# Performance work log

Measured on AMD Instinct MI355X. Metric: run time of the kernel, lower is better.

The kernel has to match this reference:

```python
import jax, jax.numpy as jnp
import numpy as np

B, S, D, H, E, O = 8, 2048, 512, 8, 64, 512  # batch, seq, d_in, heads, head_dim, out_dim
NEG_INF = -1e9  # keras Attention adds -1e9 to masked scores


def setup_inputs() -> dict:
    key = jax.random.key(0)
    kq, kk, kv, ko, kx = jax.random.split(key, 5)
    # glorot-uniform-style scale for kernel_size=1 convs (fan_in=D, fan_out=E)
    sqkv = float(np.sqrt(6.0 / (D + E)))
    so = float(np.sqrt(6.0 / (H * E + O)))
    return {
        "query": jax.random.normal(kx, (B, S, D), dtype=jnp.float32),
        "Wq": jax.random.uniform(kq, (H, D, E), jnp.float32, -sqkv, sqkv),
        "Wk": jax.random.uniform(kk, (H, D, E), jnp.float32, -sqkv, sqkv),
        "Wv": jax.random.uniform(kv, (H, D, E), jnp.float32, -sqkv, sqkv),
        "Wo": jax.random.uniform(ko, (H * E, O), jnp.float32, -so, so),
    }


def reference(query, Wq, Wk, Wv, Wo):
    # value defaults to query (self-attention). Conv1D(kernel_size=1, no bias)
    # is a per-timestep linear map; all heads batched into one einsum.
    Q = jnp.einsum('bsd,hde->bhse', query, Wq)
    K = jnp.einsum('bsd,hde->bhse', query, Wk)
    V = jnp.einsum('bsd,hde->bhse', query, Wv)
    # keras Attention(use_scale=False, causal=True): scores = Q K^T (no scale)
    scores = jnp.einsum('bhse,bhte->bhst', Q, K)
    causal = jnp.tril(jnp.ones((S, S), dtype=bool))  # [S, S]
    scores = jnp.where(causal, scores, NEG_INF)
    attn = jax.nn.softmax(scores, axis=-1)
    ctx = jnp.einsum('bhst,bhte->bhse', attn, V)  # [B, H, S, E]
    # concat heads along last axis (head-major), then 1x1 conv projection
    ctx = ctx.transpose(0, 2, 1, 3).reshape(B, S, H * E)
    return jnp.einsum('bsf,fo->bso', ctx, Wo)
```

## Files before the change

kernel.cpp:

```cpp
#include <hip/hip_runtime.h>
#include <stdint.h>

#define Bb 8
#define Ss 2048
#define Dd 512
#define Hh 8
#define Ee 64
#define Oo 512
#define Ff 512
#define Ncat 1536

typedef _Float16 half_t;
typedef __attribute__((ext_vector_type(8))) _Float16 f16x8;
typedef __attribute__((ext_vector_type(4))) float f32x4;
typedef __attribute__((ext_vector_type(16))) float f32x16;
typedef __attribute__((ext_vector_type(4))) float f4;
typedef __attribute__((ext_vector_type(4))) half_t h16x4;
typedef __attribute__((ext_vector_type(4))) unsigned int u32x4;

__device__ __forceinline__ float exp2_fast(float x) {
    float r; asm("v_exp_f32 %0, %1" : "=v"(r) : "v"(x)); return r;
}
__device__ __forceinline__ f32x16 zero16() {
    f32x16 z;
#pragma unroll
    for (int i = 0; i < 16; ++i) z[i] = 0.f;
    return z;
}
__device__ __forceinline__ void gload16(const half_t* g, half_t* l) {
    __builtin_amdgcn_global_load_lds(
        (const __attribute__((address_space(1))) void*)g,
        (__attribute__((address_space(3))) void*)l, 16, 0, 0);
}

__global__ __launch_bounds__(256) void k_cvt_x(const float* __restrict__ x,
                                               half_t* __restrict__ xh) {
    int t = blockIdx.x * 256 + threadIdx.x;
    int s = t >> 6, c = t & 63;
    int cg = c >> 3, cl = c & 7;
    const float* src = x + (size_t)s * Dd + c * 8;
    f4 v0 = *(const f4*)src;
    f4 v1 = *(const f4*)(src + 4);
    union { half_t h[8]; u32x4 u; } o;
#pragma unroll
    for (int j = 0; j < 4; ++j) { o.h[j] = (half_t)v0[j]; o.h[4 + j] = (half_t)v1[j]; }
    int cd = cg * 8 + (cl ^ (s & 7));
    *(u32x4*)(xh + (size_t)s * Dd + cd * 8) = o.u;
}

__global__ __launch_bounds__(256) void k_cvt_w(const float* __restrict__ Wq, const float* __restrict__ Wk,
                                               const float* __restrict__ Wv, const float* __restrict__ Wo,
                                               half_t* __restrict__ Wcat, half_t* __restrict__ WoT) {
    int t = blockIdx.x * 256 + threadIdx.x;
    union { half_t h[8]; u32x4 u; } o;
    if (t < Ncat * 64) {
        int n = t >> 6, dc = t & 63;
        int sel = n >> 9, h = (n >> 6) & 7, e = n & 63;
        const float* W = (sel == 0) ? Wq : (sel == 1) ? Wk : Wv;
        const float* src = W + ((size_t)h * Dd + dc * 8) * Ee + e;
#pragma unroll
        for (int j = 0; j < 8; ++j) o.h[j] = (half_t)src[(size_t)j * Ee];
        int dcs = (dc & ~7) | ((dc & 7) ^ (n & 7));
        *(u32x4*)(Wcat + (size_t)n * Dd + dcs * 8) = o.u;
    } else {
        int u2 = t - Ncat * 64;
        int oo = u2 >> 6, fc = u2 & 63;
        const float* src = Wo + (size_t)(fc * 8) * Oo + oo;
#pragma unroll
        for (int j = 0; j < 8; ++j) o.h[j] = (half_t)src[(size_t)j * Oo];
        int fcs = (fc & ~7) | ((fc & 7) ^ (oo & 7));
        *(u32x4*)(WoT + (size_t)oo * Ff + fcs * 8) = o.u;
    }
}

__global__ __launch_bounds__(256, 2) void k_qkv(const half_t* __restrict__ A,
                                                const half_t* __restrict__ Bw,
                                                half_t* __restrict__ Q,
                                                half_t* __restrict__ K,
                                                half_t* __restrict__ Vt) {
    __shared__ __attribute__((aligned(16))) half_t S[32768];

    int bid = blockIdx.x;
    int virt = (bid & 7) * 192 + (bid >> 3);
    int bm = virt / 12, bn = virt % 12;
    int m0 = bm * 128, n0 = bn * 128;

    int wave = threadIdx.x >> 6, lane = threadIdx.x & 63;
    int ar = lane & 15, kg = lane >> 4;
    int wm = wave >> 1, wn = wave & 1;
    int lr = lane >> 3, lc = lane & 7;

    f32x4 acc[4][4];
#pragma unroll
    for (int i = 0; i < 4; ++i)
#pragma unroll
        for (int j = 0; j < 4; ++j) acc[i][j] = (f32x4){0, 0, 0, 0};

#define STAGE_QKV(buf, kt)                                                                   \
    {                                                                                        \
        _Pragma("unroll")                                                                    \
        for (int i = 0; i < 4; ++i) {                                                        \
            int seg = wave * 4 + i;                                                          \
            int row = seg * 8 + lr;                                                          \
            gload16(A  + (size_t)(m0 + row) * Dd + (kt) * 64 + lc * 8,                       \
                    S + (buf) * 8192 + seg * 512);                                           \
            gload16(Bw + (size_t)(n0 + row) * Dd + (kt) * 64 + lc * 8,                       \
                    S + 16384 + (buf) * 8192 + seg * 512);                                   \
        }                                                                                    \
    }

    STAGE_QKV(0, 0);
    __syncthreads();
    int cur = 0;
    for (int kt = 0; kt < 8; ++kt) {
        if (kt < 7) STAGE_QKV(cur ^ 1, kt + 1);
        f16x8 bf[4][2];
#pragma unroll
        for (int n = 0; n < 4; ++n) {
            int row = wn * 64 + n * 16 + ar;
#pragma unroll
            for (int kh = 0; kh < 2; ++kh)
                bf[n][kh] = *(const f16x8*)&S[16384 + cur * 8192 + row * 64 + (((kg + kh * 4)) ^ (row & 7)) * 8];
        }
#pragma unroll
        for (int mi = 0; mi < 4; ++mi) {
            int row = wm * 64 + mi * 16 + ar;
            f16x8 a0 = *(const f16x8*)&S[cur * 8192 + row * 64 + ((kg)     ^ (row & 7)) * 8];
            f16x8 a1 = *(const f16x8*)&S[cur * 8192 + row * 64 + ((kg + 4) ^ (row & 7)) * 8];
#pragma unroll
            for (int n = 0; n < 4; ++n) {
                acc[mi][n] = __builtin_amdgcn_mfma_f32_16x16x32_f16(a0, bf[n][0], acc[mi][n], 0, 0, 0);
                acc[mi][n] = __builtin_amdgcn_mfma_f32_16x16x32_f16(a1, bf[n][1], acc[mi][n], 0, 0, 0);
            }
        }
        __syncthreads();
        cur ^= 1;
    }
    int sel = n0 >> 9;
    if (sel < 2) {
#pragma unroll
        for (int sn = 0; sn < 4; ++sn) {
            int nb = n0 + wn * 64 + sn * 16;
            int h = (nb >> 6) & 7, eb = nb & 63;
#pragma unroll
            for (int mi = 0; mi < 4; ++mi)
#pragma unroll
                for (int r = 0; r < 4; ++r) {
                    int sg = m0 + wm * 64 + mi * 16 + kg * 4 + r;
                    int bh = (sg >> 11) * 8 + h, sl = sg & 2047;
                    half_t val = (half_t)acc[mi][sn][r];
                    if (sel == 0) Q[((size_t)bh * Ss + sl) * Ee + eb + ar] = val;
                    else          K[((size_t)bh * Ss + sl) * Ee + eb + ar] = val;
                }
        }
    } else {
#pragma unroll
        for (int sn = 0; sn < 4; ++sn) {
            int e_loc = wn * 64 + sn * 16 + ar;
#pragma unroll
            for (int mi = 0; mi < 4; ++mi)
#pragma unroll
                for (int r = 0; r < 4; ++r) {
                    int s_loc = wm * 64 + mi * 16 + kg * 4 + r;
                    S[e_loc * 136 + s_loc] = (half_t)acc[mi][sn][r];
                }
        }
        __syncthreads();
        int b = m0 >> 11, sbase = m0 & 2047;
#pragma unroll
        for (int i = 0; i < 8; ++i) {
            int e_loc = wave * 32 + i * 4 + (lane >> 4);
            int chunk = lane & 15;
            f16x8 v = *(const f16x8*)&S[e_loc * 136 + chunk * 8];
            int h = ((n0 >> 6) + (e_loc >> 6)) & 7;
            int e_in = e_loc & 63;
            int bh = b * 8 + h;
            *(f16x8*)(Vt + ((size_t)bh * Ee + e_in) * Ss + sbase + chunk * 8) = v;
        }
    }
#undef STAGE_QKV
}

__global__ __launch_bounds__(256, 4) void k_attn(const half_t* __restrict__ Q,
                                                 const half_t* __restrict__ Kg,
                                                 const half_t* __restrict__ Vtg,
                                                 half_t* __restrict__ ctx) {
    __shared__ __attribute__((aligned(16))) half_t Klds[2][64 * 64];
    __shared__ __attribute__((aligned(16))) half_t Vlds[2][64 * 64];

    int bid = blockIdx.x;
    int xcd = bid & 7;
    int idx = bid >> 3;
    int g   = idx >> 3;
    int g0 = g & 3, j = g >> 2;
    int qb;
    switch (j) {
        case 0:  qb = 15 - g0; break;
        case 1:  qb = 8 + (g0 ^ 2); break;
        case 2:  qb = 4 + g0; break;
        default: qb = g0 ^ 1; break;
    }
    int bh  = xcd * 8 + (idx & 7);

    int wave = threadIdx.x >> 6, lane = threadIdx.x & 63;
    int ql = lane & 31, hi = lane >> 5;
    int qt32 = qb * 4 + wave;
    int qg = qt32 * 32 + ql;

    const half_t* Qb = Q   + (size_t)bh * Ss * Ee;
    const half_t* Kb = Kg  + (size_t)bh * Ss * Ee;
    const half_t* Vb = Vtg + (size_t)bh * Ee * Ss;

    const half_t* qp = Qb + (size_t)qg * Ee + hi * 8;
    f16x8 qf[4];
    const half_t l2e = (half_t)1.44269504f;
#pragma unroll
    for (int d = 0; d < 4; ++d) {
        qf[d] = *(const f16x8*)(qp + d * 16);
#pragma unroll
        for (int jj = 0; jj < 8; ++jj) qf[d][jj] *= l2e;
    }

    f32x16 ot0 = zero16(), ot1 = zero16();
    float m = -1e30f, lp = 0.f;

#define STAGE_KV(buf, kt64)                                                                 \
    {                                                                                       \
        _Pragma("unroll")                                                                   \
        for (int c = 0; c < 2; ++c) {                                                       \
            int seg = 2 * wave + c;                                                         \
            int tK = seg >> 2, dK = seg & 3;                                                \
            gload16(Kb + ((size_t)(kt64) * 64 + tK * 32 + ql) * Ee + dK * 16 + hi * 8,      \
                    &Klds[buf][seg * 512]);                                                 \
            int eh = (seg >> 1) & 1, d2 = seg & 1;                                          \
            gload16(Vb + (size_t)(eh * 32 + ql) * Ss + (kt64) * 64 + tK * 32 + d2 * 16 + hi * 8, \
                    &Vlds[buf][seg * 512]);                                                 \
        }                                                                                   \
    }

    STAGE_KV(0, 0);
    int cur = 0;
    int ktmax64 = qb * 2 + 1;
    for (int kt64 = 0; kt64 <= ktmax64; ++kt64) {
        __syncthreads();
        if (kt64 < ktmax64) STAGE_KV(cur ^ 1, kt64 + 1);
        int j0 = kt64 * 2;
        if (j0 <= qt32) {
            f32x16 s0 = zero16(), s1 = zero16();
            {
                f16x8 ka0 = *(const f16x8*)&Klds[cur][lane * 8];
                f16x8 ka1 = *(const f16x8*)&Klds[cur][512 + lane * 8];
                f16x8 ka2 = *(const f16x8*)&Klds[cur][1024 + lane * 8];
                f16x8 ka3 = *(const f16x8*)&Klds[cur][1536 + lane * 8];
                __builtin_amdgcn_s_setprio(1);
                s0 = __builtin_amdgcn_mfma_f32_32x32x16_f16(ka0, qf[0], s0, 0, 0, 0);
                s0 = __builtin_amdgcn_mfma_f32_32x32x16_f16(ka1, qf[1], s0, 0, 0, 0);
                s0 = __builtin_amdgcn_mfma_f32_32x32x16_f16(ka2, qf[2], s0, 0, 0, 0);
                s0 = __builtin_amdgcn_mfma_f32_32x32x16_f16(ka3, qf[3], s0, 0, 0, 0);
                __builtin_amdgcn_s_setprio(0);
            }
            {
                f16x8 kb0 = *(const f16x8*)&Klds[cur][2048 + lane * 8];
                f16x8 kb1 = *(const f16x8*)&Klds[cur][2560 + lane * 8];
                f16x8 kb2 = *(const f16x8*)&Klds[cur][3072 + lane * 8];
                f16x8 kb3 = *(const f16x8*)&Klds[cur][3584 + lane * 8];
                __builtin_amdgcn_s_setprio(1);
                s1 = __builtin_amdgcn_mfma_f32_32x32x16_f16(kb0, qf[0], s1, 0, 0, 0);
                s1 = __builtin_amdgcn_mfma_f32_32x32x16_f16(kb1, qf[1], s1, 0, 0, 0);
                s1 = __builtin_amdgcn_mfma_f32_32x32x16_f16(kb2, qf[2], s1, 0, 0, 0);
                s1 = __builtin_amdgcn_mfma_f32_32x32x16_f16(kb3, qf[3], s1, 0, 0, 0);
                __builtin_amdgcn_s_setprio(0);
            }
            if (j0 + 1 >= qt32) {
                int sh0 = (j0 - qt32) * 32;
                int sh1 = sh0 + 32;
#pragma unroll
                for (int r = 0; r < 16; ++r) {
                    int kloc = (r & 3) + 8 * (r >> 2) + 4 * hi;
                    if (sh0 >= 0 && kloc + sh0 > ql) s0[r] = -1e30f;
                    if (kloc + sh1 > ql)             s1[r] = -1e30f;
                }
            }
            float mt = fmaxf(s0[0], s1[0]);
#pragma unroll
            for (int r = 1; r < 16; ++r) mt = fmaxf(mt, fmaxf(s0[r], s1[r]));
            mt = fmaxf(mt, __shfl_xor(mt, 32));
            if (!__all(mt <= m + 8.0f)) {
                float mn = fmaxf(m, mt);
                float sc = exp2_fast(m - mn);
#pragma unroll
                for (int r = 0; r < 16; ++r) { ot0[r] *= sc; ot1[r] *= sc; }
                lp *= sc;
                m = mn;
            }
            float rs = 0.f;
#pragma unroll
            for (int r = 0; r < 16; ++r) { s0[r] = exp2_fast(s0[r] - m); rs += s0[r]; }
#pragma unroll
            for (int r = 0; r < 16; ++r) { s1[r] = exp2_fast(s1[r] - m); rs += s1[r]; }
            lp += rs;

            unsigned w0[8], w1[8];
#pragma unroll
            for (int mm = 0; mm < 8; ++mm) {
                asm("v_cvt_pkrtz_f16_f32 %0, %1, %2" : "=v"(w0[mm]) : "v"(s0[2 * mm]), "v"(s0[2 * mm + 1]));
                asm("v_cvt_pkrtz_f16_f32 %0, %1, %2" : "=v"(w1[mm]) : "v"(s1[2 * mm]), "v"(s1[2 * mm + 1]));
            }
            unsigned a0 = (unsigned)__shfl_xor((int)(hi ? w0[0] : w0[2]), 32);
            unsigned a1 = (unsigned)__shfl_xor((int)(hi ? w0[1] : w0[3]), 32);
            unsigned a2 = (unsigned)__shfl_xor((int)(hi ? w0[4] : w0[6]), 32);
            unsigned a3 = (unsigned)__shfl_xor((int)(hi ? w0[5] : w0[7]), 32);
            unsigned b0 = (unsigned)__shfl_xor((int)(hi ? w1[0] : w1[2]), 32);
            unsigned b1 = (unsigned)__shfl_xor((int)(hi ? w1[1] : w1[3]), 32);
            unsigned b2 = (unsigned)__shfl_xor((int)(hi ? w1[4] : w1[6]), 32);
            unsigned b3 = (unsigned)__shfl_xor((int)(hi ? w1[5] : w1[7]), 32);
            union { unsigned u[4]; f16x8 v; } pA0, pA1, pB0, pB1;
            pA0.u[0] = hi ? a0 : w0[0];  pA0.u[1] = hi ? a1 : w0[1];
            pA0.u[2] = hi ? w0[2] : a0;  pA0.u[3] = hi ? w0[3] : a1;
            pA1.u[0] = hi ? a2 : w0[4];  pA1.u[1] = hi ? a3 : w0[5];
            pA1.u[2] = hi ? w0[6] : a2;  pA1.u[3] = hi ? w0[7] : a3;
            pB0.u[0] = hi ? b0 : w1[0];  pB0.u[1] = hi ? b1 : w1[1];
            pB0.u[2] = hi ? w1[2] : b0;  pB0.u[3] = hi ? w1[3] : b1;
            pB1.u[0] = hi ? b2 : w1[4];  pB1.u[1] = hi ? b3 : w1[5];
            pB1.u[2] = hi ? w1[6] : b2;  pB1.u[3] = hi ? w1[7] : b3;

            {
                f16x8 va0 = *(const f16x8*)&Vlds[cur][lane * 8];
                f16x8 va1 = *(const f16x8*)&Vlds[cur][512 + lane * 8];
                f16x8 va2 = *(const f16x8*)&Vlds[cur][1024 + lane * 8];
                f16x8 va3 = *(const f16x8*)&Vlds[cur][1536 + lane * 8];
                __builtin_amdgcn_s_setprio(1);
                ot0 = __builtin_amdgcn_mfma_f32_32x32x16_f16(va0, pA0.v, ot0, 0, 0, 0);
                ot0 = __builtin_amdgcn_mfma_f32_32x32x16_f16(va1, pA1.v, ot0, 0, 0, 0);
                ot1 = __builtin_amdgcn_mfma_f32_32x32x16_f16(va2, pA0.v, ot1, 0, 0, 0);
                ot1 = __builtin_amdgcn_mfma_f32_32x32x16_f16(va3, pA1.v, ot1, 0, 0, 0);
                __builtin_amdgcn_s_setprio(0);
            }
            {
                f16x8 vb0 = *(const f16x8*)&Vlds[cur][2048 + lane * 8];
                f16x8 vb1 = *(const f16x8*)&Vlds[cur][2560 + lane * 8];
                f16x8 vb2 = *(const f16x8*)&Vlds[cur][3072 + lane * 8];
                f16x8 vb3 = *(const f16x8*)&Vlds[cur][3584 + lane * 8];
                __builtin_amdgcn_s_setprio(1);
                ot0 = __builtin_amdgcn_mfma_f32_32x32x16_f16(vb0, pB0.v, ot0, 0, 0, 0);
                ot0 = __builtin_amdgcn_mfma_f32_32x32x16_f16(vb1, pB1.v, ot0, 0, 0, 0);
                ot1 = __builtin_amdgcn_mfma_f32_32x32x16_f16(vb2, pB0.v, ot1, 0, 0, 0);
                ot1 = __builtin_amdgcn_mfma_f32_32x32x16_f16(vb3, pB1.v, ot1, 0, 0, 0);
                __builtin_amdgcn_s_setprio(0);
            }
        }
        cur ^= 1;
    }
#undef STAGE_KV

    float lf = lp + __shfl_xor(lp, 32);
    float inv = 1.0f / lf;
    int b = bh >> 3, h = bh & 7;
    int qs = qg & 7;
    half_t* cb = ctx + ((size_t)b * Ss + qg) * Ff;
#pragma unroll
    for (int gg = 0; gg < 4; ++gg) {
        h16x4 v0, v1;
#pragma unroll
        for (int jj = 0; jj < 4; ++jj) {
            v0[jj] = (half_t)(ot0[gg * 4 + jj] * inv);
            v1[jj] = (half_t)(ot1[gg * 4 + jj] * inv);
        }
        *(h16x4*)(cb + (h * 8 + (gg ^ qs)) * 8 + 4 * hi)       = v0;
        *(h16x4*)(cb + (h * 8 + ((gg + 4) ^ qs)) * 8 + 4 * hi) = v1;
    }
}

__global__ __launch_bounds__(256, 2) void k_proj(const half_t* __restrict__ A,
                                                 const half_t* __restrict__ Bw,
                                                 float* __restrict__ out) {
    __shared__ __attribute__((aligned(16))) half_t Ab[2][128 * 64];
    __shared__ __attribute__((aligned(16))) half_t Bbuf[2][128 * 64];

    int bid = blockIdx.x;
    int virt = (bid & 7) * 64 + (bid >> 3);
    int bm = virt >> 2, bn = virt & 3;
    int m0 = bm * 128, n0 = bn * 128;

    int wave = threadIdx.x >> 6, lane = threadIdx.x & 63;
    int ar = lane & 15, kg = lane >> 4;
    int wm = wave >> 1, wn = wave & 1;
    int lr = lane >> 3, lc = lane & 7;

    f32x4 acc[4][4];
#pragma unroll
    for (int i = 0; i < 4; ++i)
#pragma unroll
        for (int j = 0; j < 4; ++j) acc[i][j] = (f32x4){0, 0, 0, 0};

#define STAGE_PRJ(buf, kt)                                                              \
    {                                                                                   \
        _Pragma("unroll")                                                               \
        for (int i = 0; i < 4; ++i) {                                                   \
            int seg = wave * 4 + i;                                                     \
            int row = seg * 8 + lr;                                                     \
            gload16(A  + (size_t)(m0 + row) * Ff + (kt) * 64 + lc * 8, &Ab[buf][seg * 512]);   \
            gload16(Bw + (size_t)(n0 + row) * Ff + (kt) * 64 + lc * 8, &Bbuf[buf][seg * 512]); \
        }                                                                               \
    }

    STAGE_PRJ(0, 0);
    __syncthreads();
    int cur = 0;
    for (int kt = 0; kt < 8; ++kt) {
        if (kt < 7) STAGE_PRJ(cur ^ 1, kt + 1);
        f16x8 bf[4][2];
#pragma unroll
        for (int n = 0; n < 4; ++n) {
            int row = wn * 64 + n * 16 + ar;
#pragma unroll
            for (int kh = 0; kh < 2; ++kh)
                bf[n][kh] = *(const f16x8*)&Bbuf[cur][row * 64 + (((kg + kh * 4)) ^ (row & 7)) * 8];
        }
#pragma unroll
        for (int mi = 0; mi < 4; ++mi) {
            int row = wm * 64 + mi * 16 + ar;
            f16x8 a0 = *(const f16x8*)&Ab[cur][row * 64 + ((kg)     ^ (row & 7)) * 8];
            f16x8 a1 = *(const f16x8*)&Ab[cur][row * 64 + ((kg + 4) ^ (row & 7)) * 8];
#pragma unroll
            for (int n = 0; n < 4; ++n) {
                acc[mi][n] = __builtin_amdgcn_mfma_f32_16x16x32_f16(a0, bf[n][0], acc[mi][n], 0, 0, 0);
                acc[mi][n] = __builtin_amdgcn_mfma_f32_16x16x32_f16(a1, bf[n][1], acc[mi][n], 0, 0, 0);
            }
        }
        __syncthreads();
        cur ^= 1;
    }
#pragma unroll
    for (int sn = 0; sn < 4; ++sn)
#pragma unroll
        for (int mi = 0; mi < 4; ++mi)
#pragma unroll
            for (int r = 0; r < 4; ++r) {
                int sg = m0 + wm * 64 + mi * 16 + kg * 4 + r;
                out[(size_t)sg * Oo + n0 + wn * 64 + sn * 16 + ar] = acc[mi][sn][r];
            }
#undef STAGE_PRJ
}

extern "C" void kernel_launch(void* const* d_in, const int* in_sizes, int n_in,
                              void* d_out, int out_size, void* d_ws, size_t ws_size,
                              hipStream_t stream) {
    const float* x  = (const float*)d_in[0];
    const float* Wq = (const float*)d_in[1];
    const float* Wk = (const float*)d_in[2];
    const float* Wv = (const float*)d_in[3];
    const float* Wo = (const float*)d_in[4];
    float* out = (float*)d_out;

    char* ws = (char*)d_ws;
    size_t off = 0;
    half_t* xh   = (half_t*)(ws + off); off += (size_t)Bb * Ss * Dd * 2;
    half_t* Wcat = (half_t*)(ws + off); off += (size_t)Ncat * Dd * 2;
    half_t* WoT  = (half_t*)(ws + off); off += (size_t)Oo * Ff * 2;
    half_t* Qd   = (half_t*)(ws + off); off += (size_t)Bb * Hh * Ss * Ee * 2;
    half_t* Kd   = (half_t*)(ws + off); off += (size_t)Bb * Hh * Ss * Ee * 2;
    half_t* Vtd  = (half_t*)(ws + off); off += (size_t)Bb * Hh * Ss * Ee * 2;
    half_t* ctx  = (half_t*)(ws + off); off += (size_t)Bb * Ss * Ff * 2;

    k_cvt_x<<<4096, 256, 0, stream>>>(x, xh);
    k_cvt_w<<<512, 256, 0, stream>>>(Wq, Wk, Wv, Wo, Wcat, WoT);
    k_qkv<<<1536, 256, 0, stream>>>(xh, Wcat, Qd, Kd, Vtd);
    k_attn<<<1024, 256, 0, stream>>>(Qd, Kd, Vtd, ctx);
    k_proj<<<512, 256, 0, stream>>>(ctx, WoT, out);
}
```

Before: 130.7 us.

## Fuse fp32-to-fp16 input conversion into QKV GEMM and trim softmax reductions

```diff
diff --git a/kernel.cpp b/kernel.cpp
--- a/kernel.cpp
+++ b/kernel.cpp
@@ -12,6 +12,7 @@
 
 typedef _Float16 half_t;
 typedef __attribute__((ext_vector_type(8))) _Float16 f16x8;
+typedef __attribute__((ext_vector_type(2))) _Float16 h16x2;
 typedef __attribute__((ext_vector_type(4))) float f32x4;
 typedef __attribute__((ext_vector_type(16))) float f32x16;
 typedef __attribute__((ext_vector_type(4))) float f4;
@@ -32,20 +33,15 @@
         (const __attribute__((address_space(1))) void*)g,
         (__attribute__((address_space(3))) void*)l, 16, 0, 0);
 }
-
-__global__ __launch_bounds__(256) void k_cvt_x(const float* __restrict__ x,
-                                               half_t* __restrict__ xh) {
-    int t = blockIdx.x * 256 + threadIdx.x;
-    int s = t >> 6, c = t & 63;
-    int cg = c >> 3, cl = c & 7;
-    const float* src = x + (size_t)s * Dd + c * 8;
-    f4 v0 = *(const f4*)src;
-    f4 v1 = *(const f4*)(src + 4);
-    union { half_t h[8]; u32x4 u; } o;
-#pragma unroll
-    for (int j = 0; j < 4; ++j) { o.h[j] = (half_t)v0[j]; o.h[4 + j] = (half_t)v1[j]; }
-    int cd = cg * 8 + (cl ^ (s & 7));
-    *(u32x4*)(xh + (size_t)s * Dd + cd * 8) = o.u;
+__device__ __forceinline__ float dot2acc(unsigned w, float c) {
+#if __has_builtin(__builtin_amdgcn_fdot2)
+    union { unsigned u; h16x2 h; } v; v.u = w;
+    h16x2 one; one[0] = (half_t)1.0f; one[1] = (half_t)1.0f;
+    return __builtin_amdgcn_fdot2(v.h, one, c, false);
+#else
+    union { unsigned u; h16x2 h; } v; v.u = w;
+    return c + (float)v.h[0] + (float)v.h[1];
+#endif
 }
 
 __global__ __launch_bounds__(256) void k_cvt_w(const float* __restrict__ Wq, const float* __restrict__ Wk,
@@ -73,7 +69,7 @@
     }
 }
 
-__global__ __launch_bounds__(256, 2) void k_qkv(const half_t* __restrict__ A,
+__global__ __launch_bounds__(256, 2) void k_qkv(const float* __restrict__ X,
                                                 const half_t* __restrict__ Bw,
                                                 half_t* __restrict__ Q,
                                                 half_t* __restrict__ K,
@@ -89,6 +85,7 @@
     int ar = lane & 15, kg = lane >> 4;
     int wm = wave >> 1, wn = wave & 1;
     int lr = lane >> 3, lc = lane & 7;
+    int axc = lc ^ lr;
 
     f32x4 acc[4][4];
 #pragma unroll
@@ -96,24 +93,44 @@
 #pragma unroll
         for (int j = 0; j < 4; ++j) acc[i][j] = (f32x4){0, 0, 0, 0};
 
-#define STAGE_QKV(buf, kt)                                                                   \
+    f4 ra[4][2];
+
+#define LOADA(kt)                                                                            \
+    {                                                                                        \
+        _Pragma("unroll")                                                                    \
+        for (int i = 0; i < 4; ++i) {                                                        \
+            const float* src = X + (size_t)(m0 + (wave * 4 + i) * 8 + lr) * Dd + (kt) * 64 + axc * 8; \
+            ra[i][0] = *(const f4*)src;                                                      \
+            ra[i][1] = *(const f4*)(src + 4);                                                \
+        }                                                                                    \
+    }
+#define WRITEA(buf)                                                                          \
+    {                                                                                        \
+        _Pragma("unroll")                                                                    \
+        for (int i = 0; i < 4; ++i) {                                                        \
+            f16x8 h;                                                                         \
+            _Pragma("unroll")                                                                \
+            for (int j = 0; j < 4; ++j) { h[j] = (half_t)ra[i][0][j]; h[4 + j] = (half_t)ra[i][1][j]; } \
+            *(f16x8*)&S[(buf) * 8192 + (wave * 4 + i) * 512 + lane * 8] = h;                 \
+        }                                                                                    \
+    }
+#define BSTAGE(buf, kt)                                                                      \
     {                                                                                        \
         _Pragma("unroll")                                                                    \
         for (int i = 0; i < 4; ++i) {                                                        \
             int seg = wave * 4 + i;                                                          \
-            int row = seg * 8 + lr;                                                          \
-            gload16(A  + (size_t)(m0 + row) * Dd + (kt) * 64 + lc * 8,                       \
-                    S + (buf) * 8192 + seg * 512);                                           \
-            gload16(Bw + (size_t)(n0 + row) * Dd + (kt) * 64 + lc * 8,                       \
+            gload16(Bw + (size_t)(n0 + seg * 8 + lr) * Dd + (kt) * 64 + lc * 8,              \
                     S + 16384 + (buf) * 8192 + seg * 512);                                   \
         }                                                                                    \
     }
 
-    STAGE_QKV(0, 0);
+    LOADA(0);
+    BSTAGE(0, 0);
+    WRITEA(0);
     __syncthreads();
     int cur = 0;
     for (int kt = 0; kt < 8; ++kt) {
-        if (kt < 7) STAGE_QKV(cur ^ 1, kt + 1);
+        if (kt < 7) { LOADA(kt + 1); BSTAGE(cur ^ 1, kt + 1); }
         f16x8 bf[4][2];
 #pragma unroll
         for (int n = 0; n < 4; ++n) {
@@ -133,6 +150,7 @@
                 acc[mi][n] = __builtin_amdgcn_mfma_f32_16x16x32_f16(a1, bf[n][1], acc[mi][n], 0, 0, 0);
             }
         }
+        if (kt < 7) WRITEA(cur ^ 1);
         __syncthreads();
         cur ^= 1;
     }
@@ -178,7 +196,9 @@
             *(f16x8*)(Vt + ((size_t)bh * Ee + e_in) * Ss + sbase + chunk * 8) = v;
         }
     }
-#undef STAGE_QKV
+#undef LOADA
+#undef WRITEA
+#undef BSTAGE
 }
 
 __global__ __launch_bounds__(256, 4) void k_attn(const half_t* __restrict__ Q,
@@ -281,9 +301,15 @@
                     if (kloc + sh1 > ql)             s1[r] = -1e30f;
                 }
             }
-            float mt = fmaxf(s0[0], s1[0]);
-#pragma unroll
-            for (int r = 1; r < 16; ++r) mt = fmaxf(mt, fmaxf(s0[r], s1[r]));
+            float t[16];
+#pragma unroll
+            for (int r = 0; r < 16; ++r) t[r] = fmaxf(s0[r], s1[r]);
+            float u0 = fmaxf(fmaxf(t[0], t[1]), t[2]);
+            float u1 = fmaxf(fmaxf(t[3], t[4]), t[5]);
+            float u2 = fmaxf(fmaxf(t[6], t[7]), t[8]);
+            float u3 = fmaxf(fmaxf(t[9], t[10]), t[11]);
+            float u4 = fmaxf(fmaxf(t[12], t[13]), t[14]);
+            float mt = fmaxf(fmaxf(fmaxf(u0, u1), u2), fmaxf(fmaxf(u3, u4), t[15]));
             mt = fmaxf(mt, __shfl_xor(mt, 32));
             if (!__all(mt <= m + 8.0f)) {
                 float mn = fmaxf(m, mt);
@@ -293,12 +319,10 @@
                 lp *= sc;
                 m = mn;
             }
-            float rs = 0.f;
-#pragma unroll
-            for (int r = 0; r < 16; ++r) { s0[r] = exp2_fast(s0[r] - m); rs += s0[r]; }
-#pragma unroll
-            for (int r = 0; r < 16; ++r) { s1[r] = exp2_fast(s1[r] - m); rs += s1[r]; }
-            lp += rs;
+#pragma unroll
+            for (int r = 0; r < 16; ++r) s0[r] = exp2_fast(s0[r] - m);
+#pragma unroll
+            for (int r = 0; r < 16; ++r) s1[r] = exp2_fast(s1[r] - m);
 
             unsigned w0[8], w1[8];
 #pragma unroll
@@ -306,6 +330,11 @@
                 asm("v_cvt_pkrtz_f16_f32 %0, %1, %2" : "=v"(w0[mm]) : "v"(s0[2 * mm]), "v"(s0[2 * mm + 1]));
                 asm("v_cvt_pkrtz_f16_f32 %0, %1, %2" : "=v"(w1[mm]) : "v"(s1[2 * mm]), "v"(s1[2 * mm + 1]));
             }
+            float rsA = 0.f, rsB = 0.f;
+#pragma unroll
+            for (int mm = 0; mm < 8; ++mm) { rsA = dot2acc(w0[mm], rsA); rsB = dot2acc(w1[mm], rsB); }
+            lp += rsA + rsB;
+
             unsigned a0 = (unsigned)__shfl_xor((int)(hi ? w0[0] : w0[2]), 32);
             unsigned a1 = (unsigned)__shfl_xor((int)(hi ? w0[1] : w0[3]), 32);
             unsigned a2 = (unsigned)__shfl_xor((int)(hi ? w0[4] : w0[6]), 32);
@@ -455,7 +484,6 @@
 
     char* ws = (char*)d_ws;
     size_t off = 0;
-    half_t* xh   = (half_t*)(ws + off); off += (size_t)Bb * Ss * Dd * 2;
     half_t* Wcat = (half_t*)(ws + off); off += (size_t)Ncat * Dd * 2;
     half_t* WoT  = (half_t*)(ws + off); off += (size_t)Oo * Ff * 2;
     half_t* Qd   = (half_t*)(ws + off); off += (size_t)Bb * Hh * Ss * Ee * 2;
@@ -463,9 +491,8 @@
     half_t* Vtd  = (half_t*)(ws + off); off += (size_t)Bb * Hh * Ss * Ee * 2;
     half_t* ctx  = (half_t*)(ws + off); off += (size_t)Bb * Ss * Ff * 2;
 
-    k_cvt_x<<<4096, 256, 0, stream>>>(x, xh);
     k_cvt_w<<<512, 256, 0, stream>>>(Wq, Wk, Wv, Wo, Wcat, WoT);
-    k_qkv<<<1536, 256, 0, stream>>>(xh, Wcat, Qd, Kd, Vtd);
+    k_qkv<<<1536, 256, 0, stream>>>(x, Wcat, Qd, Kd, Vtd);
     k_attn<<<1024, 256, 0, stream>>>(Qd, Kd, Vtd, ctx);
     k_proj<<<512, 256, 0, stream>>>(ctx, WoT, out);
 }
```

Measured after the change: 132.3 us. Within noise of the previous version (+1.3%).
